# Optimization experiments

Hardware: AMD Instinct MI355X
Metric: run time of the kernel (lower is better)

The kernel has to match this reference:

```python
import jax, jax.numpy as jnp
import numpy as np

# Scattering2D hyperparameters (kymatio-style Morlet filter bank)
J, L, M, N = 2, 8, 224, 224
SIGMA0 = 0.8
XI0 = 3.0 * np.pi / 4.0
SLANT = 4.0 / L


def _fold(h, k):
    """Fourier-domain subsampling / filter periodization: fold and average k x k blocks."""
    if k == 1:
        return h
    Mh, Nh = h.shape[-2], h.shape[-1]
    return h.reshape(h.shape[:-2] + (k, Mh // k, k, Nh // k)).mean(axis=(-4, -2))


def _freq_grid():
    wx = (2 * np.pi * np.fft.fftfreq(M)).astype(np.float64)[:, None]
    wy = (2 * np.pi * np.fft.fftfreq(N)).astype(np.float64)[None, :]
    return wx, wy


def _morlet_hat(theta, xi, sigma):
    wx, wy = _freq_grid()
    u = np.cos(theta) * wx + np.sin(theta) * wy
    v = -np.sin(theta) * wx + np.cos(theta) * wy
    gab = np.exp(-0.5 * sigma ** 2 * ((u - xi) ** 2 + (v / SLANT) ** 2))
    gauss = np.exp(-0.5 * sigma ** 2 * (u ** 2 + (v / SLANT) ** 2))
    kappa = np.exp(-0.5 * sigma ** 2 * xi ** 2)  # zero-mean Morlet correction
    return (gab - kappa * gauss).astype(np.float32)


def _build_filters():
    psi = {}
    for j in range(J):
        f = np.stack([_morlet_hat(l * np.pi / L, XI0 / 2 ** j, SIGMA0 * 2 ** j) for l in range(L)])
        psi[j] = [_fold(f, 2 ** r) for r in range(j + 1)]  # periodized to each resolution
    wx, wy = _freq_grid()
    sig_phi = SIGMA0 * 2 ** (J - 1)
    phi0 = np.exp(-0.5 * sig_phi ** 2 * (wx ** 2 + wy ** 2)).astype(np.float32)
    phi = [_fold(phi0, 2 ** r) for r in range(J)]
    return psi, phi


PSI, PHI = _build_filters()


def _scattering(x):
    # x: (B, C, M, N) float32 -> (B, C, K, M/2^J, N/2^J), K = 1 + J*L + L^2*J*(J-1)/2
    xh = jnp.fft.fft2(x)
    s0 = jnp.fft.ifft2(_fold(xh * PHI[0], 2 ** J)).real[..., None, :, :]
    s1s, s2s = [], []
    for j1 in range(J):
        # first order: bandpass, subsample to resolution j1, modulus
        u1h = _fold(xh[..., None, :, :] * PSI[j1][0], 2 ** j1)       # (B,C,L,M/2^j1,N/2^j1)
        u1 = jnp.abs(jnp.fft.ifft2(u1h))
        u1h2 = jnp.fft.fft2(u1)
        s1s.append(jnp.fft.ifft2(_fold(u1h2 * PHI[j1], 2 ** (J - j1))).real)
        for j2 in range(j1 + 1, J):
            # second order over all (theta1, theta2) pairs, vectorized over L x L
            u2h = _fold(u1h2[..., None, :, :] * PSI[j2][j1], 2 ** (j2 - j1))  # (B,C,L,L,.,.)
            u2 = jnp.abs(jnp.fft.ifft2(u2h))
            s2 = jnp.fft.ifft2(_fold(jnp.fft.fft2(u2) * PHI[j2], 2 ** (J - j2))).real
            s2s.append(s2.reshape(s2.shape[:2] + (L * L,) + s2.shape[-2:]))
    return jnp.concatenate([s0] + s1s + s2s, axis=2)


def setup_inputs() -> dict:
    key = jax.random.key(0)
    k1, k2, _ = jax.random.split(key, 3)
    x = jax.random.normal(k1, (16, 3, M, N), dtype=jnp.float32)
    W_last = jax.random.normal(k2, (1000, 243), dtype=jnp.float32) * 0.02
    b_last = jnp.zeros((1000,), dtype=jnp.float32)
    return {"x": x, "W_last": W_last, "b_last": b_last}


def reference(x, W_last, b_last):
    s = _scattering(x)                                   # (B, 3, 81, 56, 56)
    B = s.shape[0]
    s = s.reshape(B, s.shape[1] * s.shape[2], s.shape[3], s.shape[4])  # flatten(1,2)
    g = s.max(axis=(-2, -1))                             # global max pool -> (B, 243)
    return g @ W_last.T + b_last                         # (B, 1000)
```

## Files before the change

kernel.cpp:

```cpp
#include <hip/hip_runtime.h>
#include <math.h>

#define PI_D 3.14159265358979323846

#define IMG224 50176
#define IMG112 12544
static const size_t OFF_FT224F = 0;
static const size_t OFF_FT224I = 2048;
static const size_t OFF_FT112F = 4096;
static const size_t OFF_FT112I = 6144;
static const size_t OFF_PHW    = 8600;
static const size_t OFF_PSI   = 257152;
static const size_t OFF_GK    = 1122688;
static const size_t OFF_XH    = 1126784;
static const size_t OFF_POOL  = 5943680;

__device__ inline unsigned fkey(float v) {
    int b = __float_as_int(v);
    return (b >= 0) ? ((unsigned)b | 0x80000000u) : ~(unsigned)b;
}
__device__ inline float funkey(unsigned u) {
    int b = (u & 0x80000000u) ? (int)(u & 0x7fffffffu) : (int)~u;
    return __int_as_float(b);
}
__device__ inline void cmac(float2& a, float2 z, float2 w) {
    a.x += z.x * w.x - z.y * w.y;
    a.y += z.x * w.y + z.y * w.x;
}
__device__ inline float2 cmulc(float2 v, float c, float s) {
    return make_float2(v.x * c - v.y * s, v.x * s + v.y * c);
}

struct C7 { float s; float wr[3][3]; float wi[3][3]; };
__device__ inline void ld7(const float2* __restrict__ W7, C7& c) {
    c.s = W7[0].x;
#pragma unroll
    for (int m = 1; m <= 3; ++m)
#pragma unroll
        for (int k = 1; k <= 3; ++k) {
            float2 w = W7[m * 7 + k];
            c.wr[m - 1][k - 1] = w.x;
            c.wi[m - 1][k - 1] = w.y;
        }
}
__device__ inline void dft7(const C7& c, const float2 t[7], float2 X[7]) {
    float2 a1 = make_float2(t[1].x + t[6].x, t[1].y + t[6].y);
    float2 b1 = make_float2(t[1].x - t[6].x, t[1].y - t[6].y);
    float2 a2 = make_float2(t[2].x + t[5].x, t[2].y + t[5].y);
    float2 b2 = make_float2(t[2].x - t[5].x, t[2].y - t[5].y);
    float2 a3 = make_float2(t[3].x + t[4].x, t[3].y + t[4].y);
    float2 b3 = make_float2(t[3].x - t[4].x, t[3].y - t[4].y);
    float bx = c.s * t[0].x, by = c.s * t[0].y;
    X[0] = make_float2(c.s * (t[0].x + a1.x + a2.x + a3.x),
                       c.s * (t[0].y + a1.y + a2.y + a3.y));
#pragma unroll
    for (int k = 0; k < 3; ++k) {
        float Px = c.wr[0][k] * a1.x + c.wr[1][k] * a2.x + c.wr[2][k] * a3.x;
        float Py = c.wr[0][k] * a1.y + c.wr[1][k] * a2.y + c.wr[2][k] * a3.y;
        float Qx = c.wi[0][k] * b1.x + c.wi[1][k] * b2.x + c.wi[2][k] * b3.x;
        float Qy = c.wi[0][k] * b1.y + c.wi[1][k] * b2.y + c.wi[2][k] * b3.y;
        X[k + 1] = make_float2(bx + Px - Qy, by + Py + Qx);
        X[6 - k] = make_float2(bx + Px + Qy, by + Py - Qx);
    }
}

template<int SGN>
__device__ inline void fft16(float2* x) {
    const float C8  = 0.70710678118654752f;
    const float C16 = 0.92387953251128674f;
    const float S16 = 0.38268343236508977f;
    const float sg = (float)SGN;
    float2 g[16];
#pragma unroll
    for (int b = 0; b < 4; ++b) {
        float2 x0 = x[b], x1 = x[4 + b], x2 = x[8 + b], x3 = x[12 + b];
        float2 e0 = make_float2(x0.x + x2.x, x0.y + x2.y);
        float2 e1 = make_float2(x0.x - x2.x, x0.y - x2.y);
        float2 o0 = make_float2(x1.x + x3.x, x1.y + x3.y);
        float2 o1 = make_float2(x1.x - x3.x, x1.y - x3.y);
        float2 io1 = (SGN > 0) ? make_float2(-o1.y, o1.x) : make_float2(o1.y, -o1.x);
        g[b * 4 + 0] = make_float2(e0.x + o0.x, e0.y + o0.y);
        g[b * 4 + 2] = make_float2(e0.x - o0.x, e0.y - o0.y);
        g[b * 4 + 1] = make_float2(e1.x + io1.x, e1.y + io1.y);
        g[b * 4 + 3] = make_float2(e1.x - io1.x, e1.y - io1.y);
    }
    g[5]  = cmulc(g[5],  C16,  sg * S16);
    g[6]  = cmulc(g[6],  C8,   sg * C8);
    g[7]  = cmulc(g[7],  S16,  sg * C16);
    g[9]  = cmulc(g[9],  C8,   sg * C8);
    g[10] = (SGN > 0) ? make_float2(-g[10].y, g[10].x)
                      : make_float2(g[10].y, -g[10].x);
    g[11] = cmulc(g[11], -C8,  sg * C8);
    g[13] = cmulc(g[13], S16,  sg * C16);
    g[14] = cmulc(g[14], -C8,  sg * C8);
    g[15] = cmulc(g[15], -C16, -sg * S16);
#pragma unroll
    for (int p = 0; p < 4; ++p) {
        float2 x0 = g[p], x1 = g[4 + p], x2 = g[8 + p], x3 = g[12 + p];
        float2 e0 = make_float2(x0.x + x2.x, x0.y + x2.y);
        float2 e1 = make_float2(x0.x - x2.x, x0.y - x2.y);
        float2 o0 = make_float2(x1.x + x3.x, x1.y + x3.y);
        float2 o1 = make_float2(x1.x - x3.x, x1.y - x3.y);
        float2 io1 = (SGN > 0) ? make_float2(-o1.y, o1.x) : make_float2(o1.y, -o1.x);
        x[p + 0]  = make_float2(e0.x + o0.x, e0.y + o0.y);
        x[p + 8]  = make_float2(e0.x - o0.x, e0.y - o0.y);
        x[p + 4]  = make_float2(e1.x + io1.x, e1.y + io1.y);
        x[p + 12] = make_float2(e1.x - io1.x, e1.y - io1.y);
    }
}

__global__ void k_fact(float2* o, int N1, int N2, double sign, double scale, int r2) {
    int base3 = N1 * N1 + N2 * N2 + N2 * N1;
    int total = base3 + (r2 ? 63 : 0);
    int N = N1 * N2;
    for (int i = blockIdx.x * blockDim.x + threadIdx.x; i < total; i += blockDim.x * gridDim.x) {
        double ang; double sc = 1.0;
        if (i < N1 * N1) {
            int n1 = i / N1, k1 = i % N1;
            ang = sign * 2.0 * PI_D * (double)((n1 * k1) % N1) / (double)N1;
        } else if (i < N1 * N1 + N2 * N2) {
            int j = i - N1 * N1; int n2 = j / N2, k2 = j % N2;
            ang = sign * 2.0 * PI_D * (double)((n2 * k2) % N2) / (double)N2;
            sc = scale;
        } else if (i < base3) {
            int j = i - N1 * N1 - N2 * N2; int n2 = j / N1, k1 = j % N1;
            ang = sign * 2.0 * PI_D * (double)((n2 * k1) % N) / (double)N;
        } else if (i < base3 + 49) {
            int j = i - base3; int n = j / 7, k = j % 7;
            ang = sign * 2.0 * PI_D * (double)((n * k) % 7) / 7.0;
            sc = scale;
        } else {
            int k = i - base3 - 49;
            ang = sign * 2.0 * PI_D * (double)k / 14.0;
        }
        o[i] = make_float2((float)(sc * cos(ang)), (float)(sc * sin(ang)));
    }
}

__global__ void k_psi(float* out) {
    int i = blockIdx.x * blockDim.x + threadIdx.x;
    if (i >= 16 * IMG224) return;
    int jl = i / IMG224, p = i % IMG224;
    int r = p / 224, c = p % 224;
    int j = jl >> 3, l = jl & 7;
    double fr = (r < 112) ? (double)r : (double)(r - 224);
    double fc = (c < 112) ? (double)c : (double)(c - 224);
    double wx = 2.0 * PI_D * fr / 224.0;
    double wy = 2.0 * PI_D * fc / 224.0;
    double theta = (double)l * PI_D / 8.0;
    double xi = (3.0 * PI_D / 4.0) / (double)(1 << j);
    double sg = 0.8 * (double)(1 << j);
    double ct = cos(theta), st = sin(theta);
    double u = ct * wx + st * wy;
    double v = -st * wx + ct * wy;
    double vs = v / 0.5;
    double s2 = 0.5 * sg * sg;
    double gab = exp(-s2 * ((u - xi) * (u - xi) + vs * vs));
    double gau = exp(-s2 * (u * u + vs * vs));
    double kap = exp(-s2 * xi * xi);
    out[i] = (float)(gab - kap * gau);
}

__global__ void k_zero(unsigned* gk, int n) {
    int i = blockIdx.x * blockDim.x + threadIdx.x;
    if (i < n) gk[i] = 0u;
}

template<int N1, int N2, int TA, int FOLD, int BS, bool REAL, int SGN>
__global__ __launch_bounds__(BS) void rk(
    const void* __restrict__ inBase, int inShift,
    const float* __restrict__ fltBase, int fltMask,
    const float2* __restrict__ FT, float2* __restrict__ out,
    int swzImg, int inStride, int inOff)
{
    constexpr int N = N1 * N2;
    constexpr int NIN = N * FOLD;
    constexpr int ZS = N + 2;
    constexpr int TS = N2 * (N1 + 1);
    constexpr int K1H = N1 / 2;
    __shared__ float2 Z[TA * ZS];
    __shared__ float2 T[TA * TS];
    const float2* W2 = FT + N1 * N1;
    const float2* TW = FT + N1 * N1 + N2 * N2;
    const int bx = blockIdx.x, a0 = blockIdx.y * TA, t = threadIdx.x;
    int gIn, gFlt, gOut;
    if (swzImg > 0) {
        int img = bx % swzImg, sub = bx / swzImg;
        gIn = img * inStride + inOff + (sub >> 3);
        gFlt = sub & fltMask;
        gOut = img * (gridDim.x / swzImg) + sub;
    } else if (swzImg < 0) {
        int xcd = bx & 7, loc = bx >> 3;
        int img = xcd * ((int)gridDim.x >> 4) + (loc >> 1);
        int lc = loc & 1;
        gIn = img; gFlt = lc & fltMask; gOut = img * 2 + lc;
    } else {
        gIn = bx >> inShift; gFlt = bx & fltMask; gOut = bx;
    }

    if (REAL) {
        const float* in = (const float*)inBase + (size_t)gIn * N * N;
#pragma unroll
        for (int r = 0; r < TA; ++r)
            for (int b = t; b < N; b += BS)
                Z[r * ZS + b] = make_float2(in[(size_t)(a0 + r) * N + b], 0.f);
    } else {
        const float2* in = (const float2*)inBase + (size_t)gIn * (NIN * NIN);
        const float* flt = fltBase + (size_t)gFlt * (NIN * NIN);
        const float s = 1.0f / (float)(FOLD * FOLD);
#pragma unroll
        for (int r = 0; r < TA; ++r) {
            int a = a0 + r;
            for (int b = t; b < N; b += BS) {
                float re = 0.f, im = 0.f;
#pragma unroll
                for (int i = 0; i < FOLD; ++i)
#pragma unroll
                    for (int j = 0; j < FOLD; ++j) {
                        int idx = (a + N * i) * NIN + (b + N * j);
                        float2 v = in[idx];
                        float f = flt[idx];
                        re += v.x * f; im += v.y * f;
                    }
                Z[r * ZS + b] = make_float2(re * s, im * s);
            }
        }
    }
    __syncthreads();
    for (int idx = t; idx < TA * N2 * 2; idx += BS) {
        int r = idx / (N2 * 2);
        int rem = idx % (N2 * 2);
        int n2 = rem / 2, h = rem % 2;
        float2 xx[N1];
#pragma unroll
        for (int n1 = 0; n1 < N1; ++n1) xx[n1] = Z[r * ZS + n1 * N2 + n2];
        fft16<SGN>(xx);
#pragma unroll
        for (int kk = 0; kk < K1H; ++kk) {
            int k1 = h * K1H + kk;
            float2 tw = TW[n2 * N1 + k1];
            T[r * TS + n2 * (N1 + 1) + k1] = cmulc(xx[k1], tw.x, tw.y);
        }
    }
    __syncthreads();
    {
        const float2* W7  = FT + N1 * N1 + N2 * N2 + N2 * N1;
        const float2* T14 = W7 + 49;
        for (int idx = t; idx < TA * N1; idx += BS) {
            int r = idx / N1, k1 = idx % N1;
            float2 E[7], O[7];
#pragma unroll
            for (int k = 0; k < 7; ++k) { E[k] = make_float2(0.f, 0.f); O[k] = make_float2(0.f, 0.f); }
            for (int m = 0; m < 7; ++m) {
                float2 te = T[r * TS + (2 * m) * (N1 + 1) + k1];
                float2 to = T[r * TS + (2 * m + 1) * (N1 + 1) + k1];
#pragma unroll
                for (int k = 0; k < 7; ++k) {
                    float2 w = W7[m * 7 + k];
                    cmac(E[k], te, w);
                    cmac(O[k], to, w);
                }
            }
#pragma unroll
            for (int k = 0; k < 14; ++k) {
                float2 tw = T14[k];
                float2 o_ = O[k % 7];
                float2 X = E[k % 7];
                X.x += o_.x * tw.x - o_.y * tw.y;
                X.y += o_.x * tw.y + o_.y * tw.x;
                Z[r * ZS + k1 + N1 * k] = X;
            }
        }
    }
    __syncthreads();
#pragma unroll
    for (int r = 0; r < TA; ++r) {
        float2* o = out + ((size_t)gOut * N + (a0 + r)) * N;
        for (int b = t; b < N; b += BS) o[b] = Z[r * ZS + b];
    }
}

template<int N1, int N2, int SPLIT, int BS, int SGN>
__global__ __launch_bounds__(BS) void ck1(
    const float2* __restrict__ in, const float2* __restrict__ FT, float2* __restrict__ out)
{
    constexpr int N = N1 * N2;
    constexpr int NC = N / SPLIT;
    const float2* TW = FT + N1 * N1 + N2 * N2;
    const int g = blockIdx.x / SPLIT, half = blockIdx.x % SPLIT;
    const int n2 = blockIdx.y, t = threadIdx.x;
    if (2 * t >= NC) return;
    const int b0 = 2 * t + half * NC;
    const float2* I = in + (size_t)g * N * N;
    float2 a0[16], a1[16];
#pragma unroll
    for (int n1 = 0; n1 < 16; ++n1) {
        float4 v = *reinterpret_cast<const float4*>(&I[(size_t)(n1 * N2 + n2) * N + b0]);
        a0[n1] = make_float2(v.x, v.y);
        a1[n1] = make_float2(v.z, v.w);
    }
    fft16<SGN>(a0);
    fft16<SGN>(a1);
#pragma unroll
    for (int k1 = 0; k1 < 16; ++k1) {
        float2 tw = TW[n2 * N1 + k1];
        float2 r0 = cmulc(a0[k1], tw.x, tw.y);
        float2 r1 = cmulc(a1[k1], tw.x, tw.y);
        *reinterpret_cast<float4*>(&out[((size_t)g * N + (k1 * N2 + n2)) * N + b0]) =
            make_float4(r0.x, r0.y, r1.x, r1.y);
    }
}

template<int N1, int N2, int SPLIT, int MODE, int BS>
__global__ __launch_bounds__(BS) void ck2(
    const float2* __restrict__ in, const float2* __restrict__ FT,
    float2* __restrict__ outc, float* __restrict__ outr)
{
    constexpr int N = N1 * N2;
    constexpr int NC = N / SPLIT;
    const int g = blockIdx.x / SPLIT, half = blockIdx.x % SPLIT;
    const int k1 = blockIdx.y, t = threadIdx.x;
    if (2 * t >= NC) return;
    const int b0 = 2 * t + half * NC;
    const float2* I = in + (size_t)g * N * N;
    const float2* W7  = FT + N1 * N1 + N2 * N2 + N2 * N1;
    const float2* T14 = W7 + 49;
    float2 E0[7], E1[7], O0[7], O1[7];
#pragma unroll
    for (int k = 0; k < 7; ++k) {
        E0[k] = make_float2(0.f, 0.f); E1[k] = make_float2(0.f, 0.f);
        O0[k] = make_float2(0.f, 0.f); O1[k] = make_float2(0.f, 0.f);
    }
#pragma unroll
    for (int m = 0; m < 7; ++m) {
        float4 ve = *reinterpret_cast<const float4*>(&I[(size_t)(k1 * 14 + 2 * m) * N + b0]);
        float4 vo = *reinterpret_cast<const float4*>(&I[(size_t)(k1 * 14 + 2 * m + 1) * N + b0]);
        float2 ve0 = make_float2(ve.x, ve.y), ve1 = make_float2(ve.z, ve.w);
        float2 vo0 = make_float2(vo.x, vo.y), vo1 = make_float2(vo.z, vo.w);
#pragma unroll
        for (int k = 0; k < 7; ++k) {
            float2 w = W7[m * 7 + k];
            cmac(E0[k], ve0, w); cmac(E1[k], ve1, w);
            cmac(O0[k], vo0, w); cmac(O1[k], vo1, w);
        }
    }
#pragma unroll
    for (int k = 0; k < 14; ++k) {
        float2 tw = T14[k];
        float2 r0 = E0[k % 7], r1 = E1[k % 7];
        float2 o0 = O0[k % 7], o1 = O1[k % 7];
        r0.x += o0.x * tw.x - o0.y * tw.y;
        r0.y += o0.x * tw.y + o0.y * tw.x;
        r1.x += o1.x * tw.x - o1.y * tw.y;
        r1.y += o1.x * tw.y + o1.y * tw.x;
        if (MODE == 0) {
            *reinterpret_cast<float4*>(&outc[((size_t)g * N + (k1 + N1 * k)) * N + b0]) =
                make_float4(r0.x, r0.y, r1.x, r1.y);
        } else {
            size_t o = ((size_t)g * N + (k1 + N1 * k)) * N + b0;
            outr[o]     = sqrtf(r0.x * r0.x + r0.y * r0.y);
            outr[o + 1] = sqrtf(r1.x * r1.x + r1.y * r1.y);
        }
    }
}

template<int SGN, int BS, int EPI>
__device__ inline void fft112_2d(float2* Z, const float2* __restrict__ FT, int t)
{
    constexpr int ZS = 113;
    constexpr int NCH = (112 * 16 + BS - 1) / BS;
    const float2* W2 = FT + 256;
    const float2* TW = FT + 256 + 49;
    C7 c7; ld7(W2, c7);
    for (int idx = t; idx < 112 * 7; idx += BS) {
        int r = idx % 112, n2 = idx / 112;
        float2 xx[16];
#pragma unroll
        for (int n1 = 0; n1 < 16; ++n1) xx[n1] = Z[r * ZS + n1 * 7 + n2];
        fft16<SGN>(xx);
#pragma unroll
        for (int k1 = 0; k1 < 16; ++k1) {
            float2 tw = TW[n2 * 16 + k1];
            Z[r * ZS + k1 * 7 + n2] = cmulc(xx[k1], tw.x, tw.y);
        }
    }
    __syncthreads();
    {
        float2 tv[NCH][7];
#pragma unroll
        for (int c = 0; c < NCH; ++c) {
            int idx = c * BS + t;
            if (idx < 112 * 16) {
                int r = idx >> 4, k1 = idx & 15;
#pragma unroll
                for (int m = 0; m < 7; ++m) tv[c][m] = Z[r * ZS + k1 * 7 + m];
            }
        }
        __syncthreads();
#pragma unroll
        for (int c = 0; c < NCH; ++c) {
            int idx = c * BS + t;
            if (idx < 112 * 16) {
                int r = idx >> 4, k1 = idx & 15;
                float2 X[7];
                dft7(c7, tv[c], X);
#pragma unroll
                for (int k = 0; k < 7; ++k) Z[r * ZS + k1 + 16 * k] = X[k];
            }
        }
    }
    __syncthreads();
    for (int idx = t; idx < 112 * 7; idx += BS) {
        int b = idx % 112, n2 = idx / 112;
        float2 xx[16];
#pragma unroll
        for (int n1 = 0; n1 < 16; ++n1) xx[n1] = Z[(n1 * 7 + n2) * ZS + b];
        fft16<SGN>(xx);
#pragma unroll
        for (int k1 = 0; k1 < 16; ++k1) {
            float2 tw = TW[n2 * 16 + k1];
            Z[(k1 * 7 + n2) * ZS + b] = cmulc(xx[k1], tw.x, tw.y);
        }
    }
    __syncthreads();
    {
        float2 tv[NCH][7];
#pragma unroll
        for (int c = 0; c < NCH; ++c) {
            int idx = c * BS + t;
            if (idx < 112 * 16) {
                int b = idx >> 4, k1 = idx & 15;
#pragma unroll
                for (int m = 0; m < 7; ++m) tv[c][m] = Z[(k1 * 7 + m) * ZS + b];
            }
        }
        __syncthreads();
#pragma unroll
        for (int c = 0; c < NCH; ++c) {
            int idx = c * BS + t;
            if (idx < 112 * 16) {
                int b = idx >> 4, k1 = idx & 15;
                float2 X[7];
                dft7(c7, tv[c], X);
#pragma unroll
                for (int k = 0; k < 7; ++k) {
                    Z[(k1 + 16 * k) * ZS + b] =
                        EPI ? make_float2(sqrtf(X[k].x * X[k].x + X[k].y * X[k].y), 0.f)
                            : X[k];
                }
            }
        }
    }
    __syncthreads();
}

template<int BS>
__global__ __launch_bounds__(BS) void sc2pipe(
    const float2* __restrict__ inBase, const float* __restrict__ psiBase,
    const float* __restrict__ taps, const float2* __restrict__ FTI,
    unsigned* __restrict__ gk, int slotBase, int inStride, int subShift)
{
    constexpr int ZS = 113;
    __shared__ float2 Z[112 * ZS];
    __shared__ float2 F[56 * 57];
    __shared__ float red[BS / 64];
    const int t = threadIdx.x, bx = blockIdx.x;
    const int nimg = (int)gridDim.x >> subShift;
    const int xcd = bx & 7, local = bx >> 3;
    const int img = xcd * (nimg >> 3) + (local >> subShift);
    const int sub = local & ((1 << subShift) - 1);
    const float2* in = inBase + (size_t)(img * inStride + (sub >> 3)) * (224 * 224);
    const float* flt = psiBase + (size_t)(sub & 7) * (224 * 224);
    float gw[6];
#pragma unroll
    for (int i = 0; i < 6; ++i) gw[i] = taps[i];

    for (int idx = t; idx < 112 * 112; idx += BS) {
        int a = idx / 112, b = idx % 112;
        float re = 0.f, im = 0.f;
#pragma unroll
        for (int i = 0; i < 2; ++i)
#pragma unroll
            for (int j = 0; j < 2; ++j) {
                int p = (a + 112 * i) * 224 + (b + 112 * j);
                float2 v = in[p]; float f = flt[p];
                re += v.x * f; im += v.y * f;
            }
        Z[a * ZS + b] = make_float2(re * 0.25f, im * 0.25f);
    }
    __syncthreads();

    fft112_2d<1, BS, 1>(Z, FTI, t);

    float* Ft = (float*)F;
    for (int idx = t; idx < 112 * 56; idx += BS) {
        int r = idx % 112, cp = idx / 112;
        int c0 = 2 * cp;
        float acc = gw[0] * Z[r * ZS + c0].x;
#pragma unroll
        for (int m = 1; m <= 5; ++m) {
            int cm = c0 - m; cm += (cm < 0) ? 112 : 0;
            int cq = c0 + m; cq -= (cq >= 112) ? 112 : 0;
            acc += gw[m] * (Z[r * ZS + cm].x + Z[r * ZS + cq].x);
        }
        Ft[r * 57 + cp] = acc;
    }
    __syncthreads();

    float mx = -INFINITY;
    for (int idx = t; idx < 56 * 56; idx += BS) {
        int j = idx % 56, ip = idx / 56;
        int r0 = 2 * ip;
        float acc = gw[0] * Ft[r0 * 57 + j];
#pragma unroll
        for (int m = 1; m <= 5; ++m) {
            int ra = r0 - m; ra += (ra < 0) ? 112 : 0;
            int rb = r0 + m; rb -= (rb >= 112) ? 112 : 0;
            acc += gw[m] * (Ft[ra * 57 + j] + Ft[rb * 57 + j]);
        }
        mx = fmaxf(mx, acc);
    }
    for (int off = 32; off > 0; off >>= 1) mx = fmaxf(mx, __shfl_down(mx, off, 64));
    if ((t & 63) == 0) red[t >> 6] = mx;
    __syncthreads();
    if (t == 0) {
#pragma unroll
        for (int w = 1; w < BS / 64; ++w) mx = fmaxf(mx, red[w]);
        atomicMax(&gk[img * 81 + slotBase + sub], fkey(mx));
    }
}

template<int SB, int BS>
__global__ __launch_bounds__(BS) void s1conv(
    const float* __restrict__ inBase, const float* __restrict__ taps,
    unsigned* __restrict__ gk, int slotBase, int slotShift, int slotMask)
{
    constexpr int OPB = 56 / SB;
    constexpr int IR  = 4 * OPB + 19;
    __shared__ float R2[IR][56];
    __shared__ float red[BS / 64];
    const int g = blockIdx.x, t = threadIdx.x;
    const int band = g % SB, grp = g / SB;
    const float* u = inBase + (size_t)grp * 50176;
    float gw[12];
#pragma unroll
    for (int i = 0; i < 12; ++i) gw[i] = taps[i];
    const int rbase = 4 * OPB * band - 11;
    for (int idx = t; idx < IR * 56; idx += BS) {
        int j = idx % 56, rr = idx / 56;
        int riw = rbase + rr;
        riw += (riw < 0) ? 224 : 0;
        riw -= (riw >= 224) ? 224 : 0;
        const float* row = u + riw * 224;
        int c0 = 4 * j;
        float acc = gw[0] * row[c0];
#pragma unroll
        for (int m = 1; m <= 11; ++m) {
            int cm = c0 - m; cm += (cm < 0) ? 224 : 0;
            int cq = c0 + m; cq -= (cq >= 224) ? 224 : 0;
            acc += gw[m] * (row[cm] + row[cq]);
        }
        R2[rr][j] = acc;
    }
    __syncthreads();
    float mx = -INFINITY;
    for (int idx = t; idx < OPB * 56; idx += BS) {
        int j = idx % 56, l = idx / 56;
        int base = 4 * l + 11;
        float acc = gw[0] * R2[base][j];
#pragma unroll
        for (int m = 1; m <= 11; ++m)
            acc += gw[m] * (R2[base - m][j] + R2[base + m][j]);
        mx = fmaxf(mx, acc);
    }
    for (int off = 32; off > 0; off >>= 1) mx = fmaxf(mx, __shfl_down(mx, off, 64));
    if ((t & 63) == 0) red[t >> 6] = mx;
    __syncthreads();
    if (t == 0) {
#pragma unroll
        for (int w = 1; w < BS / 64; ++w) mx = fmaxf(mx, red[w]);
        int slot = slotBase + ((grp >> slotShift) * 81) + (grp & slotMask);
        atomicMax(&gk[slot], fkey(mx));
    }
}

__global__ void k_linear(const unsigned* __restrict__ gk, const float* __restrict__ Wl,
                         const float* __restrict__ bl, float* __restrict__ out)
{
    int i = blockIdx.x * blockDim.x + threadIdx.x;
    if (i >= 16 * 1000) return;
    int b = i / 1000, o = i % 1000;
    float s = bl[o];
    for (int f = 0; f < 243; ++f)
        s += funkey(gk[b * 243 + f]) * Wl[o * 243 + f];
    out[i] = s;
}

static float g_taps[32];
static bool g_taps_init = false;
static void host_taps() {
    if (g_taps_init) return;
    const double s2 = 0.5 * 1.6 * 1.6;
    for (int m = 0; m < 16; ++m) {
        double acc = 0.0;
        for (int k = 0; k < 112; ++k) {
            double w0 = 2.0 * PI_D * (double)k / 224.0;
            double w1 = 2.0 * PI_D * (double)(k - 112) / 224.0;
            double F = 0.5 * (exp(-s2 * w0 * w0) + exp(-s2 * w1 * w1));
            acc += F * cos(2.0 * PI_D * (double)k * (double)m / 112.0);
        }
        g_taps[m] = (float)(acc / 112.0);
    }
    for (int m = 0; m < 16; ++m) {
        double acc = 0.0;
        for (int k = 0; k < 224; ++k) {
            double fr = (k < 112) ? (double)k : (double)(k - 224);
            double w = 2.0 * PI_D * fr / 224.0;
            acc += exp(-s2 * w * w) * cos(2.0 * PI_D * (double)k * (double)m / 224.0);
        }
        g_taps[16 + m] = (float)(acc / 224.0);
    }
    g_taps_init = true;
}

extern "C" void kernel_launch(void* const* d_in, const int* in_sizes, int n_in,
                              void* d_out, int out_size, void* d_ws, size_t ws_size,
                              hipStream_t stream)
{
    const float* x  = (const float*)d_in[0];
    const float* Wl = (const float*)d_in[1];
    const float* bl = (const float*)d_in[2];
    float* out = (float*)d_out;
    float* ws = (float*)d_ws;

    float2* FT224F = (float2*)(ws + OFF_FT224F);
    float2* FT224I = (float2*)(ws + OFF_FT224I);
    float2* FT112I = (float2*)(ws + OFF_FT112I);
    float* TAPS = ws + OFF_PHW;
    float* PSI0 = ws + OFF_PSI;
    float* PSI1 = ws + OFF_PSI + 8 * IMG224;
    unsigned* GK = (unsigned*)(ws + OFF_GK);
    float2* XH  = (float2*)(ws + OFF_XH);
    float* A0  = ws + OFF_POOL;
    float* A1  = A0 + 9633792;
    float* A23 = A1 + 9633792;

    host_taps();
    hipMemcpyAsync(TAPS, g_taps, 32 * sizeof(float), hipMemcpyHostToDevice, stream);
    k_fact<<<4, 256, 0, stream>>>(FT224F, 16, 14, -1.0, 1.0, 1);
    k_fact<<<4, 256, 0, stream>>>(FT224I, 16, 14,  1.0, 1.0 / 224.0, 1);
    k_fact<<<4, 256, 0, stream>>>(FT112I, 16, 7,   1.0, 1.0 / 112.0, 0);
    k_psi<<<(16 * IMG224 + 255) / 256, 256, 0, stream>>>(ws + OFF_PSI);
    k_zero<<<(3888 + 255) / 256, 256, 0, stream>>>(GK, 3888);

    rk<16, 14, 4, 1, 128, true, -1><<<dim3(48, 56), 128, 0, stream>>>(x, 0, nullptr, 0, FT224F, (float2*)A0, 0, 0, 0);
    ck1<16, 14, 2, 64, -1><<<dim3(96, 14), 64, 0, stream>>>((float2*)A0, FT224F, (float2*)A1);
    ck2<16, 14, 2, 0, 64><<<dim3(96, 16), 64, 0, stream>>>((float2*)A1, FT224F, XH, nullptr);

    s1conv<8, 256><<<48 * 8, 256, 0, stream>>>(x, TAPS + 16, GK, 0, 0, 0);

    sc2pipe<1024><<<384, 1024, 0, stream>>>(XH, PSI1, TAPS, FT112I, GK, 9, 1, 3);

    for (int c = 0; c < 4; ++c) {
        rk<16, 14, 4, 1, 128, false, 1><<<dim3(96, 56), 128, 0, stream>>>(
            XH, 1, PSI0 + (size_t)(2 * c) * IMG224, 1, FT224I, (float2*)A0, -1, 0, 0);
        ck1<16, 14, 2, 64, 1><<<dim3(192, 14), 64, 0, stream>>>((float2*)A0, FT224I, (float2*)A1);
        ck2<16, 14, 2, 1, 64><<<dim3(192, 16), 64, 0, stream>>>((float2*)A1, FT224I, nullptr, A23);
        s1conv<8, 256><<<96 * 8, 256, 0, stream>>>(A23, TAPS + 16, GK, 1 + 2 * c, 1, 1);
        rk<16, 14, 4, 1, 128, true, -1><<<dim3(96, 56), 128, 0, stream>>>(A23, 0, nullptr, 0, FT224F, (float2*)A0, 0, 0, 0);
        ck1<16, 14, 2, 64, -1><<<dim3(192, 14), 64, 0, stream>>>((float2*)A0, FT224F, (float2*)A1);
        ck2<16, 14, 2, 0, 64><<<dim3(192, 16), 64, 0, stream>>>((float2*)A1, FT224F, (float2*)A0, nullptr);
        sc2pipe<1024><<<768, 1024, 0, stream>>>((float2*)A0, PSI1, TAPS, FT112I, GK, 17 + 16 * c, 2, 4);
    }

    k_linear<<<(16000 + 255) / 256, 256, 0, stream>>>(GK, Wl, bl, out);
}
```

Measured before the change: 963.5 us.

## Pack two real images into one complex FFT and unpack via Hermitian symmetry

The forward FFT of the first-order modulus outputs now packs each pair of real images as the real and imaginary parts of one complex image. This halves the rk/ck1/ck2 grid sizes for that stage. The second-order kernel recovers each image's spectrum from the packed result using conjugate-symmetric index pairs (Z(k) and Z(-k)). The cost is an extra gathered load per sample in sc2pipe, plus more index arithmetic and a branch on the lane.

```diff
diff --git a/kernel.cpp b/kernel.cpp
--- a/kernel.cpp
+++ b/kernel.cpp
@@ -166,7 +166,7 @@
     if (i < n) gk[i] = 0u;
 }
 
-template<int N1, int N2, int TA, int FOLD, int BS, bool REAL, int SGN>
+template<int N1, int N2, int TA, int FOLD, int BS, int RMODE, int SGN>
 __global__ __launch_bounds__(BS) void rk(
     const void* __restrict__ inBase, int inShift,
     const float* __restrict__ fltBase, int fltMask,
@@ -180,7 +180,6 @@
     constexpr int K1H = N1 / 2;
     __shared__ float2 Z[TA * ZS];
     __shared__ float2 T[TA * TS];
-    const float2* W2 = FT + N1 * N1;
     const float2* TW = FT + N1 * N1 + N2 * N2;
     const int bx = blockIdx.x, a0 = blockIdx.y * TA, t = threadIdx.x;
     int gIn, gFlt, gOut;
@@ -198,12 +197,21 @@
         gIn = bx >> inShift; gFlt = bx & fltMask; gOut = bx;
     }
 
-    if (REAL) {
+    if (RMODE == 1) {
         const float* in = (const float*)inBase + (size_t)gIn * N * N;
 #pragma unroll
         for (int r = 0; r < TA; ++r)
             for (int b = t; b < N; b += BS)
                 Z[r * ZS + b] = make_float2(in[(size_t)(a0 + r) * N + b], 0.f);
+    } else if (RMODE == 2) {
+        const float* ia = (const float*)inBase + (size_t)(2 * gIn) * N * N;
+        const float* ib = ia + (size_t)N * N;
+#pragma unroll
+        for (int r = 0; r < TA; ++r)
+            for (int b = t; b < N; b += BS) {
+                size_t p = (size_t)(a0 + r) * N + b;
+                Z[r * ZS + b] = make_float2(ia[p], ib[p]);
+            }
     } else {
         const float2* in = (const float2*)inBase + (size_t)gIn * (NIN * NIN);
         const float* flt = fltBase + (size_t)gFlt * (NIN * NIN);
@@ -454,7 +462,7 @@
     __syncthreads();
 }
 
-template<int BS>
+template<int BS, int UNPACK>
 __global__ __launch_bounds__(BS) void sc2pipe(
     const float2* __restrict__ inBase, const float* __restrict__ psiBase,
     const float* __restrict__ taps, const float2* __restrict__ FTI,
@@ -469,7 +477,8 @@
     const int xcd = bx & 7, local = bx >> 3;
     const int img = xcd * (nimg >> 3) + (local >> subShift);
     const int sub = local & ((1 << subShift) - 1);
-    const float2* in = inBase + (size_t)(img * inStride + (sub >> 3)) * (224 * 224);
+    const int lc = sub >> 3;
+    const float2* in = inBase + (size_t)(img * inStride + (UNPACK ? 0 : lc)) * (224 * 224);
     const float* flt = psiBase + (size_t)(sub & 7) * (224 * 224);
     float gw[6];
 #pragma unroll
@@ -479,13 +488,28 @@
         int a = idx / 112, b = idx % 112;
         float re = 0.f, im = 0.f;
 #pragma unroll
-        for (int i = 0; i < 2; ++i)
+        for (int i = 0; i < 2; ++i) {
+            int rr = a + 112 * i;
+            int nr = (rr == 0) ? 0 : 224 - rr;
 #pragma unroll
             for (int j = 0; j < 2; ++j) {
-                int p = (a + 112 * i) * 224 + (b + 112 * j);
-                float2 v = in[p]; float f = flt[p];
-                re += v.x * f; im += v.y * f;
-            }
+                int cc = b + 112 * j;
+                int p = rr * 224 + cc;
+                float f = flt[p];
+                float vr, vi;
+                if (UNPACK) {
+                    int nc = (cc == 0) ? 0 : 224 - cc;
+                    float2 Zp = in[p];
+                    float2 Zm = in[nr * 224 + nc];
+                    if (lc == 0) { vr = 0.5f * (Zp.x + Zm.x); vi = 0.5f * (Zp.y - Zm.y); }
+                    else         { vr = 0.5f * (Zp.y + Zm.y); vi = 0.5f * (Zm.x - Zp.x); }
+                } else {
+                    float2 v = in[p];
+                    vr = v.x; vi = v.y;
+                }
+                re += vr * f; im += vi * f;
+            }
+        }
         Z[a * ZS + b] = make_float2(re * 0.25f, im * 0.25f);
     }
     __syncthreads();
@@ -649,28 +673,28 @@
     hipMemcpyAsync(TAPS, g_taps, 32 * sizeof(float), hipMemcpyHostToDevice, stream);
     k_fact<<<4, 256, 0, stream>>>(FT224F, 16, 14, -1.0, 1.0, 1);
     k_fact<<<4, 256, 0, stream>>>(FT224I, 16, 14,  1.0, 1.0 / 224.0, 1);
-    k_fact<<<4, 256, 0, stream>>>(FT112I, 16, 7,   1.0, 1.0 / 112.0, 0);
+    k_fact<<<1, 256, 0, stream>>>(FT112I, 16, 7,   1.0, 1.0 / 112.0, 0);
     k_psi<<<(16 * IMG224 + 255) / 256, 256, 0, stream>>>(ws + OFF_PSI);
     k_zero<<<(3888 + 255) / 256, 256, 0, stream>>>(GK, 3888);
 
-    rk<16, 14, 4, 1, 128, true, -1><<<dim3(48, 56), 128, 0, stream>>>(x, 0, nullptr, 0, FT224F, (float2*)A0, 0, 0, 0);
+    rk<16, 14, 4, 1, 128, 1, -1><<<dim3(48, 56), 128, 0, stream>>>(x, 0, nullptr, 0, FT224F, (float2*)A0, 0, 0, 0);
     ck1<16, 14, 2, 64, -1><<<dim3(96, 14), 64, 0, stream>>>((float2*)A0, FT224F, (float2*)A1);
     ck2<16, 14, 2, 0, 64><<<dim3(96, 16), 64, 0, stream>>>((float2*)A1, FT224F, XH, nullptr);
 
     s1conv<8, 256><<<48 * 8, 256, 0, stream>>>(x, TAPS + 16, GK, 0, 0, 0);
 
-    sc2pipe<1024><<<384, 1024, 0, stream>>>(XH, PSI1, TAPS, FT112I, GK, 9, 1, 3);
+    sc2pipe<1024, 0><<<384, 1024, 0, stream>>>(XH, PSI1, TAPS, FT112I, GK, 9, 1, 3);
 
     for (int c = 0; c < 4; ++c) {
-        rk<16, 14, 4, 1, 128, false, 1><<<dim3(96, 56), 128, 0, stream>>>(
+        rk<16, 14, 4, 1, 128, 0, 1><<<dim3(96, 56), 128, 0, stream>>>(
             XH, 1, PSI0 + (size_t)(2 * c) * IMG224, 1, FT224I, (float2*)A0, -1, 0, 0);
         ck1<16, 14, 2, 64, 1><<<dim3(192, 14), 64, 0, stream>>>((float2*)A0, FT224I, (float2*)A1);
         ck2<16, 14, 2, 1, 64><<<dim3(192, 16), 64, 0, stream>>>((float2*)A1, FT224I, nullptr, A23);
         s1conv<8, 256><<<96 * 8, 256, 0, stream>>>(A23, TAPS + 16, GK, 1 + 2 * c, 1, 1);
-        rk<16, 14, 4, 1, 128, true, -1><<<dim3(96, 56), 128, 0, stream>>>(A23, 0, nullptr, 0, FT224F, (float2*)A0, 0, 0, 0);
-        ck1<16, 14, 2, 64, -1><<<dim3(192, 14), 64, 0, stream>>>((float2*)A0, FT224F, (float2*)A1);
-        ck2<16, 14, 2, 0, 64><<<dim3(192, 16), 64, 0, stream>>>((float2*)A1, FT224F, (float2*)A0, nullptr);
-        sc2pipe<1024><<<768, 1024, 0, stream>>>((float2*)A0, PSI1, TAPS, FT112I, GK, 17 + 16 * c, 2, 4);
+        rk<16, 14, 4, 1, 128, 2, -1><<<dim3(48, 56), 128, 0, stream>>>(A23, 0, nullptr, 0, FT224F, (float2*)A0, 0, 0, 0);
+        ck1<16, 14, 2, 64, -1><<<dim3(96, 14), 64, 0, stream>>>((float2*)A0, FT224F, (float2*)A1);
+        ck2<16, 14, 2, 0, 64><<<dim3(96, 16), 64, 0, stream>>>((float2*)A1, FT224F, (float2*)A0, nullptr);
+        sc2pipe<1024, 1><<<768, 1024, 0, stream>>>((float2*)A0, PSI1, TAPS, FT112I, GK, 17 + 16 * c, 1, 4);
     }
 
     k_linear<<<(16000 + 255) / 256, 256, 0, stream>>>(GK, Wl, bl, out);
```

After: 1.366 ms. 1.42x slower.
